# Kernel tuning notes

Measured on AMD Instinct MI355X. Metric: run time of the kernel, lower is better.

## Reference

```python
import jax, jax.numpy as jnp
import numpy as np

DIM = 128          # feature dim
HID = 512          # rnn hidden dim
NC = 128           # n_comps (MLP outputs 2*NC)
N = 512            # batch
IN = 2 * DIM + 1   # rnn input size
MLP_H = 4 * HID


def setup_inputs() -> dict:
    key = jax.random.key(0)
    ks = jax.random.split(key, 16)
    s_in = 1.0 / np.sqrt(IN)
    s_h = 1.0 / np.sqrt(HID)
    s_m = 1.0 / np.sqrt(MLP_H)
    f32 = jnp.float32
    return {
        "x": jax.random.normal(ks[0], (N, DIM), f32),
        "mask": jnp.zeros((DIM,), f32),  # all dims unobserved
        # RNN layer 0 (input 2*dim+1 -> hidden)
        "W_ih0": jax.random.uniform(ks[1], (HID, IN), f32, -s_in, s_in),
        "W_hh0": jax.random.uniform(ks[2], (HID, HID), f32, -s_h, s_h),
        "b_ih0": jax.random.uniform(ks[3], (HID,), f32, -s_h, s_h),
        "b_hh0": jax.random.uniform(ks[4], (HID,), f32, -s_h, s_h),
        # RNN layer 1 (hidden -> hidden)
        "W_ih1": jax.random.uniform(ks[5], (HID, HID), f32, -s_h, s_h),
        "W_hh1": jax.random.uniform(ks[6], (HID, HID), f32, -s_h, s_h),
        "b_ih1": jax.random.uniform(ks[7], (HID,), f32, -s_h, s_h),
        "b_hh1": jax.random.uniform(ks[8], (HID,), f32, -s_h, s_h),
        # MLP: hidden -> 4*hidden -> 2*n_comps (ReLU)
        "W1": jax.random.uniform(ks[9], (MLP_H, HID), f32, -s_h, s_h),
        "b1": jax.random.uniform(ks[10], (MLP_H,), f32, -s_h, s_h),
        "W2": jax.random.uniform(ks[11], (2 * NC, MLP_H), f32, -s_m, s_m),
        "b2": jax.random.uniform(ks[12], (2 * NC,), f32, -s_m, s_m),
    }


def _log_prob(xt, means, covs):
    # xt: [N,1], means/covs: [N,NC]
    prec = jax.lax.rsqrt(jax.nn.softplus(covs))
    quad = jnp.sum((xt - means) ** 2 / (prec * prec), axis=1, keepdims=True)
    log_det = jnp.sum(jnp.log(prec), axis=1, keepdims=True)
    return -0.5 * (DIM * np.log(2.0 * np.pi) + quad) + log_det


def reference(x, mask, W_ih0, W_hh0, b_ih0, b_hh0, W_ih1, W_hh1, b_ih1, b_hh1,
              W1, b1, W2, b2):
    n = x.shape[0]
    x_o = x * mask                       # [N, DIM]
    masks = jnp.broadcast_to(mask, (n, DIM))
    # mask is all-zeros by construction -> every dim is unobserved, in order
    x_u = x                              # [N, DIM] unobserved values

    # previous unobserved value fed at each step (zeros at step 0)
    prev_seq = jnp.concatenate([jnp.zeros((n, 1), x.dtype), x_u[:, :-1]], axis=1)
    xs = (prev_seq.T[:, :, None], x_u.T[:, :, None])  # each [DIM, N, 1]

    def step(carry, inp):
        h0, h1, p, _ = carry
        prev_col, targ_col = inp
        cat = jnp.concatenate([prev_col, x_o, masks], axis=1)  # [N, 2*DIM+1]
        h0 = jnp.tanh(cat @ W_ih0.T + b_ih0 + h0 @ W_hh0.T + b_hh0)
        h1 = jnp.tanh(h0 @ W_ih1.T + b_ih1 + h1 @ W_hh1.T + b_hh1)
        o = h1                                               # [N, HID]
        hid = jax.nn.relu(o @ W1.T + b1)
        mc = hid @ W2.T + b2                                 # [N, 2*NC]
        means, covs = mc[:, :NC], mc[:, NC:]
        p = p + _log_prob(targ_col, means, covs)
        return (h0, h1, p, o), None

    init = (jnp.zeros((n, HID), x.dtype), jnp.zeros((n, HID), x.dtype),
            jnp.zeros((n, 1), x.dtype), jnp.zeros((n, HID), x.dtype))
    (h0, h1, p, o_last), _ = jax.lax.scan(step, init, xs)
    return o_last[:, None, :], p  # o: [N,1,HID], p: [N,1]
```

## Files before the change

kernel.cpp:

```cpp
#include <hip/hip_runtime.h>

typedef _Float16 f16;
typedef _Float16 f16x8 __attribute__((ext_vector_type(8)));
typedef float    f32x4 __attribute__((ext_vector_type(4)));
typedef unsigned int u32;
typedef u32 u32x4 __attribute__((ext_vector_type(4)));

#define MFMA16(a, b, c) __builtin_amdgcn_mfma_f32_16x16x32_f16((a), (b), (c), 0, 0, 0)

#define HSZ 262144
#define LOGDET_C 235.2482644923962f

__device__ __forceinline__ void ld16_s(u32x4& d, const f16* p) {
    asm volatile("global_load_dwordx4 %0, %1, off sc0 sc1" : "=v"(d) : "v"(p));
}
__device__ __forceinline__ void ldf_n(float& d, const float* p) {
    asm volatile("global_load_dword %0, %1, off" : "=v"(d) : "v"(p));
}
__device__ __forceinline__ void st2_n(f16* p, f16 v) {
    u32 u = (u32)__builtin_bit_cast(unsigned short, v);
    asm volatile("global_store_short %0, %1, off" :: "v"(p), "v"(u) : "memory");
}
__device__ __forceinline__ void st2_s(f16* p, f16 v) {
    u32 u = (u32)__builtin_bit_cast(unsigned short, v);
    asm volatile("global_store_short %0, %1, off sc0 sc1" :: "v"(p), "v"(u) : "memory");
}
__device__ __forceinline__ void sti_s(int* p, int v) {
    asm volatile("global_store_dword %0, %1, off sc0 sc1" :: "v"(p), "v"(v) : "memory");
}
__device__ __forceinline__ int ldi_s(const int* p) {
    int v;
    asm volatile("global_load_dword %0, %1, off sc0 sc1\ns_waitcnt vmcnt(0)"
                 : "=v"(v) : "v"(p) : "memory");
    return v;
}
__device__ __forceinline__ void gl16(const f16* g, char* l) {
    __builtin_amdgcn_global_load_lds(
        (const __attribute__((address_space(1))) u32*)g,
        (__attribute__((address_space(3))) u32*)l, 16, 0, 0);
}
__device__ __forceinline__ float tanh_fast(float x) {
    float e = __builtin_amdgcn_exp2f(x * 2.8853900817779268f);
    return 1.f - 2.f * __builtin_amdgcn_rcpf(e + 1.f);
}

__global__ void k_conv(const float* __restrict__ x, const float* __restrict__ mask,
                       const float* __restrict__ Wih0,
                       const float* __restrict__ b_ih0, const float* __restrict__ b_hh0,
                       const float* __restrict__ Whh0, const float* __restrict__ Wih1,
                       const float* __restrict__ Whh1, const float* __restrict__ W1,
                       const float* __restrict__ W2,
                       f16* __restrict__ A, f16* __restrict__ B1,
                       float* __restrict__ biasv,
                       f16* __restrict__ Whh0h, f16* __restrict__ Wih1h,
                       f16* __restrict__ Whh1h, f16* __restrict__ W1h,
                       f16* __restrict__ W2h, f16* __restrict__ h1all,
                       int* __restrict__ slots, int* __restrict__ xcdtab)
{
    int gid = blockIdx.x * 256 + threadIdx.x;
    {
        int c = gid >> 7, k = gid & 127;
        A[gid]  = (f16)(x[gid] * mask[k]);
        B1[gid] = (f16)Wih0[c * 257 + 1 + k];
    }
    if (gid < 512) {
        float s = b_ih0[gid] + b_hh0[gid];
        const float* wrow = Wih0 + gid * 257 + 129;
        for (int k = 0; k < 128; k++) s += mask[k] * wrow[k];
        biasv[gid] = s;
    }
    for (int i = gid; i < 262144; i += 65536) {
        Whh0h[i] = (f16)Whh0[i];
        Wih1h[i] = (f16)Wih1[i];
        Whh1h[i] = (f16)Whh1[i];
        h1all[i] = (f16)0.f;
    }
    for (int i = gid; i < 1048576; i += 65536) W1h[i] = (f16)W1[i];
    for (int i = gid; i < 524288;  i += 65536) W2h[i] = (f16)W2[i];
    if (gid < 32768) slots[gid] = 0;
    if (gid < 4096)  xcdtab[gid] = -1;
}

__global__ __launch_bounds__(256) void k_base(const f16* __restrict__ A,
                                              const f16* __restrict__ B1,
                                              const float* __restrict__ biasv,
                                              float* __restrict__ base,
                                              f16* __restrict__ h0s0)
{
    __shared__ float part[4][32][32];
    int tid = threadIdx.x;
    int w = tid >> 6, l = tid & 63;
    int R0 = (blockIdx.x >> 4) * 32, C0 = (blockIdx.x & 15) * 32;
    int lr = l & 15, hi = l >> 4;

    const f16* a0p = A  + (R0 + lr) * 128 + w * 32 + hi * 8;
    const f16* b0p = B1 + (C0 + lr) * 128 + w * 32 + hi * 8;
    f16x8 a0 = *(const f16x8*)(a0p);
    f16x8 a1 = *(const f16x8*)(a0p + 16 * 128);
    f16x8 b0 = *(const f16x8*)(b0p);
    f16x8 b1 = *(const f16x8*)(b0p + 16 * 128);
    f32x4 z = {0.f, 0.f, 0.f, 0.f};
    f32x4 acc00 = MFMA16(a0, b0, z);
    f32x4 acc01 = MFMA16(a0, b1, z);
    f32x4 acc10 = MFMA16(a1, b0, z);
    f32x4 acc11 = MFMA16(a1, b1, z);
#pragma unroll
    for (int r = 0; r < 4; r++) {
        part[w][hi * 4 + r][lr]           = acc00[r];
        part[w][hi * 4 + r][16 + lr]      = acc01[r];
        part[w][16 + hi * 4 + r][lr]      = acc10[r];
        part[w][16 + hi * 4 + r][16 + lr] = acc11[r];
    }
    __syncthreads();
    int rr = tid >> 3, c0 = (tid & 7) * 4;
    int gr = R0 + rr;
#pragma unroll
    for (int cc = 0; cc < 4; cc++) {
        int gc = C0 + c0 + cc;
        float s = part[0][rr][c0 + cc] + part[1][rr][c0 + cc] +
                  part[2][rr][c0 + cc] + part[3][rr][c0 + cc] + biasv[gc];
        base[gr * 512 + gc] = s;
        h0s0[gr * 512 + gc] = (f16)tanh_fast(s);
    }
}

#define LDH(off, f) (*(const f16x8*)((char*)Wl + (off) + (f) * 2048 + hbase))
#define LDB(m, f)   (*(const f16x8*)((char*)Wl + (m) * 32768 + (f) * 2048 + wbase))

#define RNN_STAGED(ST2x)                                                      \
    for (int p = 0; p < 128; p++) {                                           \
        const f16* H0 = h0all + (size_t)(p & PMASK) * HSZ;                    \
        const f16* H1 = h1all + (size_t)p * HSZ;                              \
        f16* H1o = h1all + (size_t)(p + 1) * HSZ;                             \
        f16* H0o = h0all + (size_t)((p + 1) & PMASK) * HSZ;                   \
        float xprev[4];                                                       \
        _Pragma("unroll")                                                     \
        for (int r = 0; r < 4; r++) ldf_n(xprev[r], x + (outrow + r) * 128 + p); \
        if (p) __syncthreads();      \
        if (p) { int v; for (;;) { v = ldi_s(pollA); if (__all(v >= p)) break; \
                                   __builtin_amdgcn_s_sleep(1); } }           \
        _Pragma("unroll")                                                     \
        for (int i = 0; i < 8; i++) {                                         \
            int c = w + i * 4, f = c >> 1, rg = c & 1;                        \
            gl16(H1 + (size_t)(R0 + rg * 16 + (l >> 2)) * 512 + f * 32 + (l & 3) * 8, \
                 (char*)Wl + OFF_H1S + f * 2048 + rg * 1024);                 \
        }                                                                     \
        if (p) { int v; for (;;) { v = ldi_s(pollB); if (__all(v >= p)) break; \
                                   __builtin_amdgcn_s_sleep(1); } }           \
        _Pragma("unroll")                                                     \
        for (int i = 0; i < 8; i++) {                                         \
            int c = w + i * 4, f = c >> 1, rg = c & 1;                        \
            gl16(H0 + (size_t)(R0 + rg * 16 + (l >> 2)) * 512 + f * 32 + (l & 3) * 8, \
                 (char*)Wl + OFF_H0S + f * 2048 + rg * 1024);                 \
        }                                                                     \
        asm volatile("s_waitcnt vmcnt(0)" ::: "memory");                      \
        __syncthreads();                                                      \
        f32x4 z4 = {0.f, 0.f, 0.f, 0.f};                                      \
        f32x4 a0a = z4, a0b = z4;                                             \
        _Pragma("unroll")                                                     \
        for (int f = 0; f < 16; f += 2) {                                     \
            a0a = MFMA16(LDH(OFF_H0S, f),     bW0[f],     a0a);               \
            a0b = MFMA16(LDH(OFF_H0S, f + 1), bW0[f + 1], a0b);               \
        }                                                                     \
        f32x4 acc0 = a0a + a0b;                                               \
        _Pragma("unroll")                                                     \
        for (int r = 0; r < 4; r++) {                                         \
            f16 v0 = (f16)tanh_fast(acc0[r] + basef[r] + xprev[r] * w0);      \
            ST2x(H0o + (outrow + r) * 512 + outcolg, v0);                     \
        }                                                                     \
        f32x4 a1a = z4, a1b = z4;                                             \
        _Pragma("unroll")                                                     \
        for (int f = 0; f < 16; f += 2) {                                     \
            a1a = MFMA16(LDH(OFF_H0S, f),     LDB(0, f),     a1a);            \
            a1b = MFMA16(LDH(OFF_H0S, f + 1), LDB(0, f + 1), a1b);            \
        }                                                                     \
        _Pragma("unroll")                                                     \
        for (int f = 0; f < 16; f += 2) {                                     \
            a1a = MFMA16(LDH(OFF_H1S, f),     LDB(1, f),     a1a);            \
            a1b = MFMA16(LDH(OFF_H1S, f + 1), LDB(1, f + 1), a1b);            \
        }                                                                     \
        asm volatile("s_waitcnt vmcnt(0)" ::: "memory");                      \
        if (l == 0) sti_s(myB, p + 1);                                        \
        f32x4 acc1 = a1a + a1b;                                               \
        _Pragma("unroll")                                                     \
        for (int r = 0; r < 4; r++) {                                         \
            f16 v1 = (f16)tanh_fast(acc1[r] + bsum);                          \
            ST2x(H1o + (outrow + r) * 512 + outcolg, v1);                     \
        }                                                                     \
        asm volatile("s_waitcnt vmcnt(0)" ::: "memory");                      \
        if (l == 0) sti_s(myA, p + 1);                                        \
    }

#define RNN_DIRECT()                                                          \
    for (int p = 0; p < 128; p++) {                                           \
        const f16* H0 = h0all + (size_t)(p & PMASK) * HSZ;                    \
        const f16* H1 = h1all + (size_t)p * HSZ;                              \
        const f16* ap = H0 + (R0 + r_lo + lr) * 512 + hi * 8;                 \
        const f16* bp = H1 + (R0 + r_lo + lr) * 512 + hi * 8;                 \
        f16* H1o = h1all + (size_t)(p + 1) * HSZ;                             \
        f16* H0o = h0all + (size_t)((p + 1) & PMASK) * HSZ;                   \
        float xprev[4];                                                       \
        _Pragma("unroll")                                                     \
        for (int r = 0; r < 4; r++) ldf_n(xprev[r], x + (outrow + r) * 128 + p); \
        if (p) { int v; for (;;) { v = ldi_s(pollB); if (__all(v >= p)) break; \
                                   __builtin_amdgcn_s_sleep(1); } }           \
        u32x4 ra0[16], ra1[16];                                               \
        __builtin_amdgcn_sched_barrier(0);                                    \
        _Pragma("unroll")                                                     \
        for (int f = 0; f < 16; f++) ld16_s(ra0[f], ap + f * 32);             \
        asm volatile("s_waitcnt vmcnt(0)" ::: "memory");                      \
        __builtin_amdgcn_sched_barrier(0);                                    \
        f32x4 z4 = {0.f, 0.f, 0.f, 0.f};                                      \
        f32x4 a0a = z4, a0b = z4, a1a = z4, a1b = z4;                         \
        _Pragma("unroll")                                                     \
        for (int f = 0; f < 16; f += 2) {                                     \
            f16x8 A0 = __builtin_bit_cast(f16x8, ra0[f]);                     \
            f16x8 A1 = __builtin_bit_cast(f16x8, ra0[f + 1]);                 \
            a0a = MFMA16(A0, bW0[f],     a0a);                                \
            a0b = MFMA16(A1, bW0[f + 1], a0b);                                \
            a1a = MFMA16(A0, LDB(0, f),     a1a);                             \
            a1b = MFMA16(A1, LDB(0, f + 1), a1b);                             \
        }                                                                     \
        f32x4 acc0 = a0a + a0b;                                               \
        _Pragma("unroll")                                                     \
        for (int r = 0; r < 4; r++) {                                         \
            f16 v0 = (f16)tanh_fast(acc0[r] + basef[r] + xprev[r] * w0);      \
            st2_s(H0o + (outrow + r) * 512 + outcolg, v0);                    \
        }                                                                     \
        asm volatile("s_waitcnt vmcnt(0)" ::: "memory");                      \
        if (l == 0) sti_s(myB, p + 1);                                        \
        if (p) { int v; for (;;) { v = ldi_s(pollA); if (__all(v >= p)) break; \
                                   __builtin_amdgcn_s_sleep(1); } }           \
        __builtin_amdgcn_sched_barrier(0);                                    \
        _Pragma("unroll")                                                     \
        for (int f = 0; f < 16; f++) ld16_s(ra1[f], bp + f * 32);             \
        asm volatile("s_waitcnt vmcnt(0)" ::: "memory");                      \
        __builtin_amdgcn_sched_barrier(0);                                    \
        _Pragma("unroll")                                                     \
        for (int f = 0; f < 16; f += 2) {                                     \
            a1a = MFMA16(__builtin_bit_cast(f16x8, ra1[f]),     LDB(1, f),     a1a); \
            a1b = MFMA16(__builtin_bit_cast(f16x8, ra1[f + 1]), LDB(1, f + 1), a1b); \
        }                                                                     \
        f32x4 acc1 = a1a + a1b;                                               \
        _Pragma("unroll")                                                     \
        for (int r = 0; r < 4; r++) {                                         \
            f16 v1 = (f16)tanh_fast(acc1[r] + bsum);                          \
            st2_s(H1o + (outrow + r) * 512 + outcolg, v1);                    \
        }                                                                     \
        asm volatile("s_waitcnt vmcnt(0)" ::: "memory");                      \
        if (l == 0) sti_s(myA, p + 1);                                        \
    }

template<bool H0F>
__global__ __launch_bounds__(256, 1) void k_rnn(
    f16* __restrict__ h0all, f16* __restrict__ h1all,
    const f16* __restrict__ Whh0h, const f16* __restrict__ Wih1h,
    const f16* __restrict__ Whh1h,
    const float* __restrict__ base, const float* __restrict__ x,
    const float* __restrict__ Wih0, const float* __restrict__ b_ih1,
    const float* __restrict__ b_hh1, int* __restrict__ slots,
    int* __restrict__ xcdtab)
{
    constexpr int PMASK = H0F ? 255 : 1;
    const int OFF_H0S = 65536, OFF_H1S = 98304;
    __shared__ __align__(16) char Wl[131072];
    __shared__ int s_fast;
    int tid = threadIdx.x;
    int w = tid >> 6, l = tid & 63;
    int bid = blockIdx.x;
    int sub = (bid >> 3) & 1, cj = bid >> 4;
    int cluster = (bid & 7) * 2 + sub;
    int R0 = cluster * 32, C0 = cj * 32;

    int xcdreg;
    asm("s_getreg_b32 %0, hwreg(20, 0, 4)" : "=s"(xcdreg));
    int my_xcd = xcdreg & 7;
    if (H0F && tid == 0) sti_s(xcdtab + (cluster * 16 + cj) * 16, my_xcd);

    {
        const f16* srcs[2] = { Wih1h, Whh1h };
        for (int ch = tid; ch < 4096; ch += 256) {
            int m = ch >> 11, c2 = ch & 2047;
            int col = c2 >> 6, f = (c2 >> 2) & 15, hh = c2 & 3;
            f16x8 v = *(const f16x8*)(srcs[m] + (size_t)(C0 + col) * 512 +
                                      f * 32 + hh * 8);
            *(f16x8*)((char*)Wl + m * 32768 + f * 2048 + col * 64 + hh * 16) = v;
        }
    }
    __syncthreads();

    int lr = l & 15, hi = l >> 4;
    int r_lo = (w >> 1) * 16, c_lo = (w & 1) * 16;
    int outrow = R0 + r_lo + hi * 4;
    int outcolg = C0 + c_lo + lr;
    int hbase = (r_lo + lr) * 64 + hi * 16;
    int wbase = (c_lo + lr) * 64 + hi * 16;

    f16x8 bW0[16];
    {
        const f16* w0p = Whh0h + (size_t)outcolg * 512 + hi * 8;
#pragma unroll
        for (int f = 0; f < 16; f++) bW0[f] = *(const f16x8*)(w0p + f * 32);
    }

    float basef[4];
#pragma unroll
    for (int r = 0; r < 4; r++) basef[r] = base[(outrow + r) * 512 + outcolg];
    float w0 = Wih0[outcolg * 257];
    float bsum = b_ih1[outcolg] + b_hh1[outcolg];

    int* slotA = slots;
    int* slotB = slots + 16384;
    int wslot = cj * 4 + w;
    int* myA = slotA + (cluster * 64 + wslot) * 16;
    int* myB = slotB + (cluster * 64 + wslot) * 16;
    const int* pollA = slotA + (cluster * 64 + l) * 16;
    const int* pollB = slotB + (cluster * 64 + l) * 16;

    bool fast = false;
    if constexpr (H0F) {
        if (w == 0) {
            int v;
            for (;;) {
                v = (l < 16) ? ldi_s(xcdtab + (cluster * 16 + l) * 16) : 0;
                if (!__any(l < 16 && v == -1)) break;
                __builtin_amdgcn_s_sleep(1);
            }
            int f = __all(l >= 16 || v == my_xcd);
            if (l == 0) s_fast = f;
        }
        __syncthreads();
        fast = (s_fast != 0);
    } else {
        if (tid == 0) s_fast = 0;
        __syncthreads();
    }

    if (H0F && fast) {
        RNN_STAGED(st2_n)
    } else if (H0F) {
        RNN_STAGED(st2_s)
    } else {
        RNN_DIRECT()
    }
}
#undef LDH
#undef LDB

__global__ __launch_bounds__(512, 2) void k_phaseB(const f16* __restrict__ h1all,
                                                   const f16* __restrict__ W1h,
                                                   const f16* __restrict__ W2h,
                                                   const float* __restrict__ b1v,
                                                   const float* __restrict__ b2,
                                                   const float* __restrict__ x,
                                                   float* __restrict__ pcontrib)
{
    __shared__ __align__(16) char Wl[108544];
    const int OFF_W2 = 65536, OFF_HID = 98304;

    int tid = threadIdx.x;
    int wv = tid >> 6, l = tid & 63;
    int lr = l & 15, hi = l >> 4;
    int M0 = blockIdx.x * 128;

    const f16* Hrow = h1all + HSZ + (size_t)(M0 + wv * 16 + lr) * 512;
    f16x8 afrag[16];
#pragma unroll
    for (int ks = 0; ks < 16; ks++)
        afrag[ks] = *(const f16x8*)(Hrow + ks * 32 + hi * 8);

    f32x4 mc[16] = {};

    {
#pragma unroll
        for (int it = 0; it < 4; it++) {
            int idx = it * 512 + tid;
            gl16(W1h + (size_t)(idx & 31) * 512 + (idx >> 5) * 8,
                 Wl + idx * 16);
        }
#pragma unroll
        for (int it = 0; it < 2; it++) {
            int idx = it * 512 + tid;
            gl16(W2h + (size_t)(idx & 255) * 2048 + (idx >> 8) * 8,
                 Wl + OFF_W2 + idx * 16);
        }
    }

    for (int c = 0; c < 64; c++) {
        int p = c & 1;
        __syncthreads();

        if (c + 1 < 64) {
            const int nc = (c + 1) * 32, q = p ^ 1;
#pragma unroll
            for (int it = 0; it < 4; it++) {
                int idx = it * 512 + tid;
                gl16(W1h + (size_t)(nc + (idx & 31)) * 512 + (idx >> 5) * 8,
                     Wl + q * 32768 + idx * 16);
            }
#pragma unroll
            for (int it = 0; it < 2; it++) {
                int idx = it * 512 + tid;
                gl16(W2h + (size_t)(idx & 255) * 2048 + nc + (idx >> 8) * 8,
                     Wl + OFF_W2 + q * 16384 + idx * 16);
            }
        }

        {
            f32x4 s3a = {0.f, 0.f, 0.f, 0.f}, s3b = s3a;
#pragma unroll
            for (int ks = 0; ks < 16; ks++) {
                f16x8 wb0 = *(const f16x8*)(Wl + p * 32768 +
                                            ((ks * 4 + hi) * 32 + lr) * 16);
                f16x8 wb1 = *(const f16x8*)(Wl + p * 32768 +
                                            ((ks * 4 + hi) * 32 + 16 + lr) * 16);
                s3a = MFMA16(afrag[ks], wb0, s3a);
                s3b = MFMA16(afrag[ks], wb1, s3b);
            }
            float bb0 = b1v[c * 32 + lr];
            float bb1 = b1v[c * 32 + 16 + lr];
#pragma unroll
            for (int r = 0; r < 4; r++) {
                int lrow = wv * 16 + hi * 4 + r;
                *(f16*)(Wl + OFF_HID + (lrow * 40 + lr) * 2) =
                    (f16)fmaxf(s3a[r] + bb0, 0.f);
                *(f16*)(Wl + OFF_HID + (lrow * 40 + 16 + lr) * 2) =
                    (f16)fmaxf(s3b[r] + bb1, 0.f);
            }
        }
        __syncthreads();

        {
            f16x8 a = *(const f16x8*)(Wl + OFF_HID +
                                      ((wv * 16 + lr) * 40 + hi * 8) * 2);
#pragma unroll
            for (int cf = 0; cf < 16; cf++) {
                f16x8 b = *(const f16x8*)(Wl + OFF_W2 + p * 16384 +
                                          (hi * 256 + cf * 16 + lr) * 16);
                mc[cf] = MFMA16(a, b, mc[cf]);
            }
        }
    }

    float quad[4] = {}, ls[4] = {}, xt[4];
#pragma unroll
    for (int r = 0; r < 4; r++) {
        int m = M0 + wv * 16 + hi * 4 + r;
        xt[r] = x[(m & 511) * 128 + (m >> 9)];
    }
#pragma unroll
    for (int cf = 0; cf < 8; cf++) {
        int cc = cf * 16 + lr;
        float bm = b2[cc], bc = b2[128 + cc];
#pragma unroll
        for (int r = 0; r < 4; r++) {
            float mean = mc[cf][r] + bm;
            float cov  = mc[cf + 8][r] + bc;
            float sp = log1pf(expf(-fabsf(cov))) + fmaxf(cov, 0.f);
            float d = xt[r] - mean;
            quad[r] += d * d * sp;
            ls[r] += logf(sp);
        }
    }
#pragma unroll
    for (int mm = 1; mm < 16; mm <<= 1)
#pragma unroll
        for (int r = 0; r < 4; r++) {
            quad[r] += __shfl_xor(quad[r], mm, 64);
            ls[r]   += __shfl_xor(ls[r], mm, 64);
        }
    if (lr == 0) {
#pragma unroll
        for (int r = 0; r < 4; r++) {
            int m = M0 + wv * 16 + hi * 4 + r;
            pcontrib[m] = -0.5f * (LOGDET_C + quad[r]) - 0.5f * ls[r];
        }
    }
}

__global__ void k_fin(const f16* __restrict__ h1last,
                      const float* __restrict__ pcontrib, float* __restrict__ out)
{
    int gid = blockIdx.x * 256 + threadIdx.x;
    for (int i = gid; i < HSZ; i += 131072) out[i] = (float)h1last[i];
    if (gid < 512) {
        float s = 0.f;
        for (int tt = 0; tt < 128; tt++) s += pcontrib[tt * 512 + gid];
        out[HSZ + gid] = s;
    }
}

extern "C" void kernel_launch(void* const* d_in, const int* in_sizes, int n_in,
                              void* d_out, int out_size, void* d_ws, size_t ws_size,
                              hipStream_t stream) {
    const float* x     = (const float*)d_in[0];
    const float* mask  = (const float*)d_in[1];
    const float* Wih0  = (const float*)d_in[2];
    const float* Whh0  = (const float*)d_in[3];
    const float* b_ih0 = (const float*)d_in[4];
    const float* b_hh0 = (const float*)d_in[5];
    const float* Wih1  = (const float*)d_in[6];
    const float* Whh1  = (const float*)d_in[7];
    const float* b_ih1 = (const float*)d_in[8];
    const float* b_hh1 = (const float*)d_in[9];
    const float* W1    = (const float*)d_in[10];
    const float* b1    = (const float*)d_in[11];
    const float* W2    = (const float*)d_in[12];
    const float* b2    = (const float*)d_in[13];

    char* ws = (char*)d_ws;
    size_t off = 0;
    auto take = [&](size_t bytes) { char* p = ws + off; off += (bytes + 255) & ~(size_t)255; return p; };
    float* base    = (float*)take(512 * 512 * 4);
    f16* Whh0h     = (f16*)take(HSZ * 2);
    f16* Wih1h     = (f16*)take(HSZ * 2);
    f16* Whh1h     = (f16*)take(HSZ * 2);
    f16* W1h       = (f16*)take(1048576 * 2);
    f16* W2h       = (f16*)take(524288 * 2);
    f16* h0buf     = (f16*)take(2 * HSZ * 2);
    f16* h1all     = (f16*)take((size_t)129 * HSZ * 2);
    float* pcontrib= (float*)take(128 * 512 * 4);
    f16* A         = (f16*)take(65536 * 2);
    f16* B1        = (f16*)take(65536 * 2);
    float* biasv   = (float*)take(512 * 4);
    int* slots     = (int*)take(32768 * 4);
    int* xcdtab    = (int*)take(4096 * 4);
    if (off > ws_size) return;

    const size_t h0all_bytes = (size_t)129 * HSZ * 2;
    bool big = (off + h0all_bytes + 256 <= ws_size);
    f16* h0all = big ? (f16*)take(h0all_bytes) : h0buf;

    k_conv<<<256, 256, 0, stream>>>(x, mask, Wih0, b_ih0, b_hh0, Whh0, Wih1, Whh1,
                                    W1, W2, A, B1, biasv, Whh0h, Wih1h, Whh1h,
                                    W1h, W2h, h1all, slots, xcdtab);
    k_base<<<256, 256, 0, stream>>>(A, B1, biasv, base, h0all);
    if (big)
        k_rnn<true><<<256, 256, 0, stream>>>(h0all, h1all, Whh0h, Wih1h, Whh1h,
                                             base, x, Wih0, b_ih1, b_hh1, slots,
                                             xcdtab);
    else
        k_rnn<false><<<256, 256, 0, stream>>>(h0all, h1all, Whh0h, Wih1h, Whh1h,
                                              base, x, Wih0, b_ih1, b_hh1, slots,
                                              xcdtab);
    k_phaseB<<<512, 512, 0, stream>>>(h1all, W1h, W2h, b1, b2, x, pcontrib);
    k_fin<<<512, 256, 0, stream>>>(h1all + (size_t)128 * HSZ, pcontrib, (float*)d_out);
}
```

Before: 830.8 us.

## Reorder RNN step to overlap layer-1 wait with layer-0 work; swizzle LDS layout

Each RNN step now waits only on the h0 dependency first, stages h0, and computes the layer-0 output and the W_ih1·h0 partial product in one interleaved loop, so the h0 fragments are read from LDS once for both. It signals its layer-B slot before polling for h1 readiness and staging h1, which lets cross-block waits overlap with useful work. The LDS layout for staged h and the cached weights is changed so each lane's 16-byte fragment is contiguous by lane index, to reduce bank conflicts. In exchange it adds an extra barrier and vmcnt wait per step, and it depends on the new synchronisation order being free of deadlock.

```diff
diff --git a/kernel.cpp b/kernel.cpp
--- a/kernel.cpp
+++ b/kernel.cpp
@@ -124,8 +124,8 @@
     }
 }
 
-#define LDH(off, f) (*(const f16x8*)((char*)Wl + (off) + (f) * 2048 + hbase))
-#define LDB(m, f)   (*(const f16x8*)((char*)Wl + (m) * 32768 + (f) * 2048 + wbase))
+#define LDH(off, f) (*(const f16x8*)((char*)Wl + (off) + (f) * 2048 + hgb))
+#define LDB(m, f)   (*(const f16x8*)((char*)Wl + (m) * 32768 + (f) * 2048 + wgb))
 
 #define RNN_STAGED(ST2x)                                                      \
     for (int p = 0; p < 128; p++) {                                           \
@@ -136,31 +136,26 @@
         float xprev[4];                                                       \
         _Pragma("unroll")                                                     \
         for (int r = 0; r < 4; r++) ldf_n(xprev[r], x + (outrow + r) * 128 + p); \
-        if (p) __syncthreads();      \
-        if (p) { int v; for (;;) { v = ldi_s(pollA); if (__all(v >= p)) break; \
-                                   __builtin_amdgcn_s_sleep(1); } }           \
-        _Pragma("unroll")                                                     \
-        for (int i = 0; i < 8; i++) {                                         \
-            int c = w + i * 4, f = c >> 1, rg = c & 1;                        \
-            gl16(H1 + (size_t)(R0 + rg * 16 + (l >> 2)) * 512 + f * 32 + (l & 3) * 8, \
-                 (char*)Wl + OFF_H1S + f * 2048 + rg * 1024);                 \
-        }                                                                     \
         if (p) { int v; for (;;) { v = ldi_s(pollB); if (__all(v >= p)) break; \
                                    __builtin_amdgcn_s_sleep(1); } }           \
         _Pragma("unroll")                                                     \
         for (int i = 0; i < 8; i++) {                                         \
-            int c = w + i * 4, f = c >> 1, rg = c & 1;                        \
-            gl16(H0 + (size_t)(R0 + rg * 16 + (l >> 2)) * 512 + f * 32 + (l & 3) * 8, \
-                 (char*)Wl + OFF_H0S + f * 2048 + rg * 1024);                 \
+            int c = w + i * 4, f = c >> 1, g = c & 1;                         \
+            gl16(H0 + (size_t)(R0 + g * 16 + (l & 15)) * 512 + f * 32 + (l >> 4) * 8, \
+                 (char*)Wl + OFF_H0S + f * 2048 + g * 1024);                  \
         }                                                                     \
         asm volatile("s_waitcnt vmcnt(0)" ::: "memory");                      \
         __syncthreads();                                                      \
         f32x4 z4 = {0.f, 0.f, 0.f, 0.f};                                      \
-        f32x4 a0a = z4, a0b = z4;                                             \
+        f32x4 a0a = z4, a0b = z4, a1a = z4, a1b = z4;                         \
         _Pragma("unroll")                                                     \
         for (int f = 0; f < 16; f += 2) {                                     \
-            a0a = MFMA16(LDH(OFF_H0S, f),     bW0[f],     a0a);               \
-            a0b = MFMA16(LDH(OFF_H0S, f + 1), bW0[f + 1], a0b);               \
+            f16x8 A0 = LDH(OFF_H0S, f);                                       \
+            f16x8 A1 = LDH(OFF_H0S, f + 1);                                   \
+            a0a = MFMA16(A0, bW0[f],     a0a);                                \
+            a0b = MFMA16(A1, bW0[f + 1], a0b);                                \
+            a1a = MFMA16(A0, LDB(0, f),     a1a);                             \
+            a1b = MFMA16(A1, LDB(0, f + 1), a1b);                             \
         }                                                                     \
         f32x4 acc0 = a0a + a0b;                                               \
         _Pragma("unroll")                                                     \
@@ -168,19 +163,23 @@
             f16 v0 = (f16)tanh_fast(acc0[r] + basef[r] + xprev[r] * w0);      \
             ST2x(H0o + (outrow + r) * 512 + outcolg, v0);                     \
         }                                                                     \
-        f32x4 a1a = z4, a1b = z4;                                             \
-        _Pragma("unroll")                                                     \
-        for (int f = 0; f < 16; f += 2) {                                     \
-            a1a = MFMA16(LDH(OFF_H0S, f),     LDB(0, f),     a1a);            \
-            a1b = MFMA16(LDH(OFF_H0S, f + 1), LDB(0, f + 1), a1b);            \
-        }                                                                     \
+        asm volatile("s_waitcnt vmcnt(0)" ::: "memory");                      \
+        if (l == 0) sti_s(myB, p + 1);                                        \
+        if (p) { int v; for (;;) { v = ldi_s(pollA); if (__all(v >= p)) break; \
+                                   __builtin_amdgcn_s_sleep(1); } }           \
+        _Pragma("unroll")                                                     \
+        for (int i = 0; i < 8; i++) {                                         \
+            int c = w + i * 4, f = c >> 1, g = c & 1;                         \
+            gl16(H1 + (size_t)(R0 + g * 16 + (l & 15)) * 512 + f * 32 + (l >> 4) * 8, \
+                 (char*)Wl + OFF_H1S + f * 2048 + g * 1024);                  \
+        }                                                                     \
+        asm volatile("s_waitcnt vmcnt(0)" ::: "memory");                      \
+        __syncthreads();                                                      \
         _Pragma("unroll")                                                     \
         for (int f = 0; f < 16; f += 2) {                                     \
             a1a = MFMA16(LDH(OFF_H1S, f),     LDB(1, f),     a1a);            \
             a1b = MFMA16(LDH(OFF_H1S, f + 1), LDB(1, f + 1), a1b);            \
         }                                                                     \
-        asm volatile("s_waitcnt vmcnt(0)" ::: "memory");                      \
-        if (l == 0) sti_s(myB, p + 1);                                        \
         f32x4 acc1 = a1a + a1b;                                               \
         _Pragma("unroll")                                                     \
         for (int r = 0; r < 4; r++) {                                         \
@@ -281,10 +280,11 @@
         const f16* srcs[2] = { Wih1h, Whh1h };
         for (int ch = tid; ch < 4096; ch += 256) {
             int m = ch >> 11, c2 = ch & 2047;
-            int col = c2 >> 6, f = (c2 >> 2) & 15, hh = c2 & 3;
+            int f = c2 >> 7, col = (c2 >> 2) & 31, hh = c2 & 3;
             f16x8 v = *(const f16x8*)(srcs[m] + (size_t)(C0 + col) * 512 +
                                       f * 32 + hh * 8);
-            *(f16x8*)((char*)Wl + m * 32768 + f * 2048 + col * 64 + hh * 16) = v;
+            *(f16x8*)((char*)Wl + m * 32768 + f * 2048 + (col >> 4) * 1024 +
+                      (hh * 16 + (col & 15)) * 16) = v;
         }
     }
     __syncthreads();
@@ -293,8 +293,8 @@
     int r_lo = (w >> 1) * 16, c_lo = (w & 1) * 16;
     int outrow = R0 + r_lo + hi * 4;
     int outcolg = C0 + c_lo + lr;
-    int hbase = (r_lo + lr) * 64 + hi * 16;
-    int wbase = (c_lo + lr) * 64 + hi * 16;
+    int hgb = (w >> 1) * 1024 + l * 16;
+    int wgb = (w & 1) * 1024 + l * 16;
 
     f16x8 bW0[16];
     {
```

Result: slower. 887.0 us (+6.8%).
